# Kernel optimization log

Measured on AMD Instinct MI355X. Metric: run time of the kernel, lower is better.

## Reference

```python
import jax, jax.numpy as jnp
import numpy as np

PI = jnp.float32(3.14159265359)  # same truncated constant as the torch source
LOG_2PI = jnp.log(2.0 * PI)
STAB = 0.001  # covariance stabilizer added before inversion in the original


def _decoder(z, W1, b1, W2, b2, W3, b3, W4, b4):
    # f: Linear(z_dim,64)-ELU-Linear(64,128)-ELU-Linear(128,256)-ELU-Linear(256,784)-Sigmoid
    h = jax.nn.elu(z @ W1.T + b1)
    h = jax.nn.elu(h @ W2.T + b2)
    h = jax.nn.elu(h @ W3.T + b3)
    return jax.nn.sigmoid(h @ W4.T + b4)


def setup_inputs() -> dict:
    key = jax.random.key(0)
    ks = jax.random.split(key, 6)
    N, K, D, Z = 512, 256, 784, 2

    def lin(k, fan_in, fan_out):
        k1, k2 = jax.random.split(k)
        lim = 1.0 / np.sqrt(fan_in)
        W = jax.random.uniform(k1, (fan_out, fan_in), minval=-lim, maxval=lim, dtype=jnp.float32)
        b = jax.random.uniform(k2, (fan_out,), minval=-lim, maxval=lim, dtype=jnp.float32)
        return W, b

    W1, b1 = lin(ks[0], Z, 64)
    W2, b2 = lin(ks[1], 64, 128)
    W3, b3 = lin(ks[2], 128, 256)
    W4, b4 = lin(ks[3], 256, D)
    X = jax.random.uniform(ks[4], (N, D), dtype=jnp.float32)   # image pixels in [0,1)
    z = jax.random.normal(ks[5], (K, Z), dtype=jnp.float32)    # latent MC samples
    log_std = jnp.zeros((1,), dtype=jnp.float32)               # self.log_std_ = tensor([0.0])
    return dict(X=X, z=z, log_std=log_std, W1=W1, b1=b1, W2=W2, b2=b2,
                W3=W3, b3=b3, W4=W4, b4=b4)


def reference(X, z, log_std, W1, b1, W2, b2, W3, b3, W4, b4):
    # expected_log_likelihood(X, z) == objective(X, z, variational=False)
    N, D = X.shape
    K, Z = z.shape
    s = jnp.exp(log_std[0])  # isotropic likelihood variance (covariance = s * I_D)

    # --- log_likelihood: MVN log-prob with covariance s*I_D (closed form of det/inverse) ---
    params = _decoder(z, W1, b1, W2, b2, W3, b3, W4, b4)           # (K, D)
    diffs = X[:, None, :] - params[None, :, :]                      # (N, K, D) dominant traffic
    quad = jnp.sum(diffs * diffs, axis=-1) / (s + STAB)             # inv((s+eps)*I) = I/(s+eps)
    log_norm = -0.5 * D * LOG_2PI - 0.5 * (D * log_std[0])          # log det(s*I_D) = D*log s
    ll = log_norm - 0.5 * quad                                      # (N, K)

    # --- log_prior: MVN log-prob with identity covariance (stabilized inverse: I/1.001) ---
    log_prior = -0.5 * Z * LOG_2PI - 0.5 * jnp.sum(z * z, axis=-1) / (1.0 + STAB)  # (K,)

    # --- importance weights computed under no_grad in the original ---
    sg = jax.lax.stop_gradient
    ll_c = sg(ll)
    lp_c = sg(log_prior)
    m = jnp.max(ll_c)
    ll_s = ll_c - m                                                 # (N, K)
    log_joint_s = ll_s + lp_c[None, :]                              # (N, K)
    evidence_s = jnp.exp(ll_s).sum(axis=-1) / K                     # (N,)
    log_evidence_s = jnp.log(evidence_s)
    log_posteriors = (log_joint_s - log_evidence_s[:, None]).T      # (K, N)
    iw = jnp.exp(log_posteriors - lp_c[:, None])                    # (K, N), constants

    ell = (iw.T * ll).sum(axis=-1) / K                              # (N,)
    return ell.sum() / N
```

## Files before the change

kernel.cpp:

```cpp
#include <hip/hip_runtime.h>
#include <math.h>

#define LOG_2PI 1.8378770664093453f

__device__ __forceinline__ float elu_f(float x) {
    return x > 0.0f ? x : expm1f(x);
}
__device__ __forceinline__ float sigmoid_f(float x) {
    return 1.0f / (1.0f + expf(-x));
}

__global__ __launch_bounds__(256) void decoder_kernel(
    const float* __restrict__ z,
    const float* __restrict__ W1, const float* __restrict__ b1,
    const float* __restrict__ W2, const float* __restrict__ b2,
    const float* __restrict__ W3, const float* __restrict__ b3,
    const float* __restrict__ W4, const float* __restrict__ b4,
    float* __restrict__ PT)
{
    __shared__ __align__(16) float h1[4][64];
    __shared__ __align__(16) float h2[4][128];
    __shared__ __align__(16) float h3[4][256];

    const int t  = threadIdx.x;
    const int kt = blockIdx.x >> 2;
    const int jq = blockIdx.x & 3;
    const int k0 = kt * 4;

    {
        int kl = t >> 6, o = t & 63;
        float z0 = z[(k0 + kl) * 2 + 0];
        float z1 = z[(k0 + kl) * 2 + 1];
        float v = fmaf(z0, W1[o * 2 + 0], fmaf(z1, W1[o * 2 + 1], b1[o]));
        h1[kl][o] = elu_f(v);
    }
    __syncthreads();

    for (int idx = t; idx < 512; idx += 256) {
        int kl = idx >> 7, o = idx & 127;
        const float4* wr = reinterpret_cast<const float4*>(W2 + o * 64);
        const float4* hr = reinterpret_cast<const float4*>(h1[kl]);
        float acc = b2[o];
        #pragma unroll
        for (int i = 0; i < 16; ++i) {
            float4 w = wr[i]; float4 a = hr[i];
            acc = fmaf(w.x, a.x, acc); acc = fmaf(w.y, a.y, acc);
            acc = fmaf(w.z, a.z, acc); acc = fmaf(w.w, a.w, acc);
        }
        h2[kl][o] = elu_f(acc);
    }
    __syncthreads();

    for (int idx = t; idx < 1024; idx += 256) {
        int kl = idx >> 8, o = idx & 255;
        const float4* wr = reinterpret_cast<const float4*>(W3 + o * 128);
        const float4* hr = reinterpret_cast<const float4*>(h2[kl]);
        float acc = b3[o];
        #pragma unroll
        for (int i = 0; i < 32; ++i) {
            float4 w = wr[i]; float4 a = hr[i];
            acc = fmaf(w.x, a.x, acc); acc = fmaf(w.y, a.y, acc);
            acc = fmaf(w.z, a.z, acc); acc = fmaf(w.w, a.w, acc);
        }
        h3[kl][o] = elu_f(acc);
    }
    __syncthreads();

    if (t < 196) {
        const int j = jq * 196 + t;
        const float4* wr = reinterpret_cast<const float4*>(W4 + j * 256);
        const float4* h0 = reinterpret_cast<const float4*>(h3[0]);
        const float4* hA = reinterpret_cast<const float4*>(h3[1]);
        const float4* hB = reinterpret_cast<const float4*>(h3[2]);
        const float4* hC = reinterpret_cast<const float4*>(h3[3]);
        float bb = b4[j];
        float a0 = bb, a1 = bb, a2 = bb, a3 = bb;
        #pragma unroll 8
        for (int i = 0; i < 64; ++i) {
            float4 w = wr[i];
            float4 x0 = h0[i], x1 = hA[i], x2 = hB[i], x3 = hC[i];
            a0 = fmaf(w.x, x0.x, a0); a0 = fmaf(w.y, x0.y, a0);
            a0 = fmaf(w.z, x0.z, a0); a0 = fmaf(w.w, x0.w, a0);
            a1 = fmaf(w.x, x1.x, a1); a1 = fmaf(w.y, x1.y, a1);
            a1 = fmaf(w.z, x1.z, a1); a1 = fmaf(w.w, x1.w, a1);
            a2 = fmaf(w.x, x2.x, a2); a2 = fmaf(w.y, x2.y, a2);
            a2 = fmaf(w.z, x2.z, a2); a2 = fmaf(w.w, x2.w, a2);
            a3 = fmaf(w.x, x3.x, a3); a3 = fmaf(w.y, x3.y, a3);
            a3 = fmaf(w.z, x3.z, a3); a3 = fmaf(w.w, x3.w, a3);
        }
        float4 r = make_float4(sigmoid_f(a0), sigmoid_f(a1),
                               sigmoid_f(a2), sigmoid_f(a3));
        *reinterpret_cast<float4*>(PT + j * 256 + k0) = r;
    }
}

__global__ __launch_bounds__(256) void quad_part_kernel(
    const float* __restrict__ X, const float* __restrict__ log_std,
    const float* __restrict__ PT, float* __restrict__ part)
{
    __shared__ __align__(16) float Xs[8 * 784];

    const int t  = threadIdx.x;
    const int nb = blockIdx.x >> 2;
    const int bq = blockIdx.x & 3;
    const int n0 = nb * 8;

    {
        const float4* X4  = reinterpret_cast<const float4*>(X + n0 * 784);
        float4*       Xs4 = reinterpret_cast<float4*>(Xs);
        for (int i = t; i < 1568; i += 256) Xs4[i] = X4[i];
    }
    __syncthreads();

    const int w  = t >> 6, l = t & 63;
    const int rl = 2 * w + (l >> 5);
    const int dh = (l >> 4) & 1;
    const int kv = l & 15;

    const float4* P4   = reinterpret_cast<const float4*>(PT) + bq * 16 + kv;
    const float*  xrow = Xs + rl * 784 + dh * 392;
    const int     dofs = dh * 392;

    float ax = 0.0f, ay = 0.0f, az = 0.0f, aw = 0.0f;
    #pragma unroll 4
    for (int d = 0; d < 392; ++d) {
        float4 p = P4[(dofs + d) * 64];
        float x = xrow[d];
        float d0 = x - p.x, d1 = x - p.y, d2 = x - p.z, d3 = x - p.w;
        ax = fmaf(d0, d0, ax); ay = fmaf(d1, d1, ay);
        az = fmaf(d2, d2, az); aw = fmaf(d3, d3, aw);
    }

    ax += __shfl_xor(ax, 16); ay += __shfl_xor(ay, 16);
    az += __shfl_xor(az, 16); aw += __shfl_xor(aw, 16);

    float ls  = log_std[0];
    float s   = expf(ls);
    float inv = 1.0f / (s + 0.001f);
    float log_norm = -0.5f * 784.0f * LOG_2PI - 0.5f * 784.0f * ls;

    float ll0 = log_norm - 0.5f * ax * inv;
    float ll1 = log_norm - 0.5f * ay * inv;
    float ll2 = log_norm - 0.5f * az * inv;
    float ll3 = log_norm - 0.5f * aw * inv;

    float m = fmaxf(fmaxf(ll0, ll1), fmaxf(ll2, ll3));
    for (int off = 1; off < 16; off <<= 1)
        m = fmaxf(m, __shfl_xor(m, off));

    float e0 = expf(ll0 - m), e1 = expf(ll1 - m);
    float e2 = expf(ll2 - m), e3 = expf(ll3 - m);
    float s0 = (e0 + e1) + (e2 + e3);
    float s1 = fmaf(e0, ll0, fmaf(e1, ll1, fmaf(e2, ll2, e3 * ll3)));
    for (int off = 1; off < 16; off <<= 1) {
        s0 += __shfl_xor(s0, off);
        s1 += __shfl_xor(s1, off);
    }

    if ((l & 31) == 0) {
        int row = n0 + rl;
        float* pp = part + (row * 4 + bq) * 3;
        pp[0] = m; pp[1] = s0; pp[2] = s1;
    }
}

__global__ __launch_bounds__(256) void finalize_kernel(
    const float* __restrict__ part, float* __restrict__ out)
{
    __shared__ float red[4];
    const int t = threadIdx.x;
    float v = 0.0f;
    #pragma unroll
    for (int h = 0; h < 2; ++h) {
        const float* pp = part + (t + h * 256) * 12;
        float M = fmaxf(fmaxf(pp[0], pp[3]), fmaxf(pp[6], pp[9]));
        float S0 = 0.0f, S1 = 0.0f;
        #pragma unroll
        for (int q = 0; q < 4; ++q) {
            float f = expf(pp[q * 3] - M);
            S0 = fmaf(pp[q * 3 + 1], f, S0);
            S1 = fmaf(pp[q * 3 + 2], f, S1);
        }
        v += S1 / S0;
    }
    for (int off = 32; off > 0; off >>= 1)
        v += __shfl_down(v, off);
    if ((t & 63) == 0) red[t >> 6] = v;
    __syncthreads();
    if (t == 0)
        out[0] = (red[0] + red[1] + red[2] + red[3]) * (1.0f / 512.0f);
}

extern "C" void kernel_launch(void* const* d_in, const int* in_sizes, int n_in,
                              void* d_out, int out_size, void* d_ws, size_t ws_size,
                              hipStream_t stream) {
    const float* X       = (const float*)d_in[0];
    const float* z       = (const float*)d_in[1];
    const float* log_std = (const float*)d_in[2];
    const float* W1      = (const float*)d_in[3];
    const float* b1      = (const float*)d_in[4];
    const float* W2      = (const float*)d_in[5];
    const float* b2      = (const float*)d_in[6];
    const float* W3      = (const float*)d_in[7];
    const float* b3      = (const float*)d_in[8];
    const float* W4      = (const float*)d_in[9];
    const float* b4      = (const float*)d_in[10];
    float* out = (float*)d_out;

    float* wsf  = (float*)d_ws;
    float* PT   = wsf;
    float* part = wsf + 200704;

    decoder_kernel<<<256, 256, 0, stream>>>(z, W1, b1, W2, b2, W3, b3, W4, b4, PT);
    quad_part_kernel<<<256, 256, 0, stream>>>(X, log_std, PT, part);
    finalize_kernel<<<1, 256, 0, stream>>>(part, out);
}
```

Measured before the change: 131.8 us.

## Register-tile 4 rows x 4 samples per thread in quad kernel, split D across warps

Each thread now accumulates a 4x4 tile (4 X rows by 4 latent samples), so every loaded float4 of decoder output is reused across four rows instead of one. The D dimension is split across the four warps and four lane groups and combined through shuffles and a shared-memory reduction. The grid doubles to 512 blocks of 4 rows each. This cuts global loads of PT per FLOP and raises parallelism, at the cost of more registers, an extra sync, and a cross-warp reduction.

```diff
diff --git a/kernel.cpp b/kernel.cpp
--- a/kernel.cpp
+++ b/kernel.cpp
@@ -98,69 +98,101 @@
     const float* __restrict__ X, const float* __restrict__ log_std,
     const float* __restrict__ PT, float* __restrict__ part)
 {
-    __shared__ __align__(16) float Xs[8 * 784];
+    __shared__ __align__(16) float Xs[4][784];
+    __shared__ float red[4][16][17];
 
     const int t  = threadIdx.x;
-    const int nb = blockIdx.x >> 2;
-    const int bq = blockIdx.x & 3;
-    const int n0 = nb * 8;
+    const int nb = blockIdx.x & 127;
+    const int bq = blockIdx.x >> 7;
+    const int n0 = nb * 4;
 
     {
         const float4* X4  = reinterpret_cast<const float4*>(X + n0 * 784);
-        float4*       Xs4 = reinterpret_cast<float4*>(Xs);
-        for (int i = t; i < 1568; i += 256) Xs4[i] = X4[i];
-    }
-    __syncthreads();
-
-    const int w  = t >> 6, l = t & 63;
-    const int rl = 2 * w + (l >> 5);
-    const int dh = (l >> 4) & 1;
-    const int kv = l & 15;
-
-    const float4* P4   = reinterpret_cast<const float4*>(PT) + bq * 16 + kv;
-    const float*  xrow = Xs + rl * 784 + dh * 392;
-    const int     dofs = dh * 392;
-
-    float ax = 0.0f, ay = 0.0f, az = 0.0f, aw = 0.0f;
-    #pragma unroll 4
-    for (int d = 0; d < 392; ++d) {
-        float4 p = P4[(dofs + d) * 64];
-        float x = xrow[d];
-        float d0 = x - p.x, d1 = x - p.y, d2 = x - p.z, d3 = x - p.w;
-        ax = fmaf(d0, d0, ax); ay = fmaf(d1, d1, ay);
-        az = fmaf(d2, d2, az); aw = fmaf(d3, d3, aw);
-    }
-
-    ax += __shfl_xor(ax, 16); ay += __shfl_xor(ay, 16);
-    az += __shfl_xor(az, 16); aw += __shfl_xor(aw, 16);
-
-    float ls  = log_std[0];
-    float s   = expf(ls);
-    float inv = 1.0f / (s + 0.001f);
-    float log_norm = -0.5f * 784.0f * LOG_2PI - 0.5f * 784.0f * ls;
-
-    float ll0 = log_norm - 0.5f * ax * inv;
-    float ll1 = log_norm - 0.5f * ay * inv;
-    float ll2 = log_norm - 0.5f * az * inv;
-    float ll3 = log_norm - 0.5f * aw * inv;
-
-    float m = fmaxf(fmaxf(ll0, ll1), fmaxf(ll2, ll3));
-    for (int off = 1; off < 16; off <<= 1)
-        m = fmaxf(m, __shfl_xor(m, off));
-
-    float e0 = expf(ll0 - m), e1 = expf(ll1 - m);
-    float e2 = expf(ll2 - m), e3 = expf(ll3 - m);
-    float s0 = (e0 + e1) + (e2 + e3);
-    float s1 = fmaf(e0, ll0, fmaf(e1, ll1, fmaf(e2, ll2, e3 * ll3)));
-    for (int off = 1; off < 16; off <<= 1) {
-        s0 += __shfl_xor(s0, off);
-        s1 += __shfl_xor(s1, off);
-    }
-
-    if ((l & 31) == 0) {
-        int row = n0 + rl;
-        float* pp = part + (row * 4 + bq) * 3;
-        pp[0] = m; pp[1] = s0; pp[2] = s1;
+        float4*       Xs4 = reinterpret_cast<float4*>(&Xs[0][0]);
+        for (int i = t; i < 784; i += 256) Xs4[i] = X4[i];
+    }
+    __syncthreads();
+
+    const int w    = t >> 6, l = t & 63;
+    const int kv   = l & 15;
+    const int dsub = l >> 4;
+    const int db   = w * 196 + dsub * 49;
+
+    const float4* P4 = reinterpret_cast<const float4*>(PT) + bq * 16 + kv;
+
+    float a00=0.f,a01=0.f,a02=0.f,a03=0.f;
+    float a10=0.f,a11=0.f,a12=0.f,a13=0.f;
+    float a20=0.f,a21=0.f,a22=0.f,a23=0.f;
+    float a30=0.f,a31=0.f,a32=0.f,a33=0.f;
+
+    #pragma unroll 7
+    for (int i = 0; i < 49; ++i) {
+        const int d = db + i;
+        float4 p = P4[d * 64];
+        float x0 = Xs[0][d], x1 = Xs[1][d], x2 = Xs[2][d], x3 = Xs[3][d];
+        float e;
+        e = x0-p.x; a00=fmaf(e,e,a00);  e = x0-p.y; a01=fmaf(e,e,a01);
+        e = x0-p.z; a02=fmaf(e,e,a02);  e = x0-p.w; a03=fmaf(e,e,a03);
+        e = x1-p.x; a10=fmaf(e,e,a10);  e = x1-p.y; a11=fmaf(e,e,a11);
+        e = x1-p.z; a12=fmaf(e,e,a12);  e = x1-p.w; a13=fmaf(e,e,a13);
+        e = x2-p.x; a20=fmaf(e,e,a20);  e = x2-p.y; a21=fmaf(e,e,a21);
+        e = x2-p.z; a22=fmaf(e,e,a22);  e = x2-p.w; a23=fmaf(e,e,a23);
+        e = x3-p.x; a30=fmaf(e,e,a30);  e = x3-p.y; a31=fmaf(e,e,a31);
+        e = x3-p.z; a32=fmaf(e,e,a32);  e = x3-p.w; a33=fmaf(e,e,a33);
+    }
+
+    #define RED2(v) v += __shfl_xor(v, 16); v += __shfl_xor(v, 32);
+    RED2(a00) RED2(a01) RED2(a02) RED2(a03)
+    RED2(a10) RED2(a11) RED2(a12) RED2(a13)
+    RED2(a20) RED2(a21) RED2(a22) RED2(a23)
+    RED2(a30) RED2(a31) RED2(a32) RED2(a33)
+    #undef RED2
+
+    if (l < 16) {
+        float* rr = red[w][l];
+        rr[0]=a00;  rr[1]=a01;  rr[2]=a02;  rr[3]=a03;
+        rr[4]=a10;  rr[5]=a11;  rr[6]=a12;  rr[7]=a13;
+        rr[8]=a20;  rr[9]=a21;  rr[10]=a22; rr[11]=a23;
+        rr[12]=a30; rr[13]=a31; rr[14]=a32; rr[15]=a33;
+    }
+    __syncthreads();
+
+    if (l < 16) {
+        const int r4 = w * 4;
+        float q0 = red[0][l][r4+0] + red[1][l][r4+0] + red[2][l][r4+0] + red[3][l][r4+0];
+        float q1 = red[0][l][r4+1] + red[1][l][r4+1] + red[2][l][r4+1] + red[3][l][r4+1];
+        float q2 = red[0][l][r4+2] + red[1][l][r4+2] + red[2][l][r4+2] + red[3][l][r4+2];
+        float q3 = red[0][l][r4+3] + red[1][l][r4+3] + red[2][l][r4+3] + red[3][l][r4+3];
+
+        float ls  = log_std[0];
+        float s   = expf(ls);
+        float inv = 1.0f / (s + 0.001f);
+        float log_norm = -0.5f * 784.0f * LOG_2PI - 0.5f * 784.0f * ls;
+
+        float ll0 = log_norm - 0.5f * q0 * inv;
+        float ll1 = log_norm - 0.5f * q1 * inv;
+        float ll2 = log_norm - 0.5f * q2 * inv;
+        float ll3 = log_norm - 0.5f * q3 * inv;
+
+        float m = fmaxf(fmaxf(ll0, ll1), fmaxf(ll2, ll3));
+        #pragma unroll
+        for (int off = 1; off < 16; off <<= 1)
+            m = fmaxf(m, __shfl_xor(m, off));
+
+        float e0 = expf(ll0 - m), e1 = expf(ll1 - m);
+        float e2 = expf(ll2 - m), e3 = expf(ll3 - m);
+        float s0 = (e0 + e1) + (e2 + e3);
+        float s1 = fmaf(e0, ll0, fmaf(e1, ll1, fmaf(e2, ll2, e3 * ll3)));
+        #pragma unroll
+        for (int off = 1; off < 16; off <<= 1) {
+            s0 += __shfl_xor(s0, off);
+            s1 += __shfl_xor(s1, off);
+        }
+
+        if (l == 0) {
+            float* pp = part + ((n0 + w) * 4 + bq) * 3;
+            pp[0] = m; pp[1] = s0; pp[2] = s1;
+        }
     }
 }
 
@@ -212,6 +244,6 @@
     float* part = wsf + 200704;
 
     decoder_kernel<<<256, 256, 0, stream>>>(z, W1, b1, W2, b2, W3, b3, W4, b4, PT);
-    quad_part_kernel<<<256, 256, 0, stream>>>(X, log_std, PT, part);
+    quad_part_kernel<<<512, 256, 0, stream>>>(X, log_std, PT, part);
     finalize_kernel<<<1, 256, 0, stream>>>(part, out);
 }
```

Result: faster. 116.2 us (median of 2 runs) (-11.8%).
